# Kernel optimization log

Hardware: AMD Instinct MI355X
Metric: run time of the kernel (lower is better)

Reference implementation:

```python
import jax, jax.numpy as jnp
import numpy as np

D_IN, D, BOX, REL, THR = 2048, 512, 8, 80, 0.5

def _ln(x, g, b):
    m = jnp.mean(x, -1, keepdims=True)
    v = jnp.mean((x - m) ** 2, -1, keepdims=True)
    return (x - m) * jax.lax.rsqrt(v + 1e-5) * g + b

def setup_inputs():
    key = jax.random.key(0)
    ks = jax.random.split(key, 24)
    B, N = 32, 50
    def lin(k, i, o):
        return jax.random.normal(k, (i, o), jnp.float32) / np.sqrt(i)
    z = lambda n: jnp.zeros((n,), jnp.float32)
    o = lambda n: jnp.ones((n,), jnp.float32)
    return {
        "images": jax.random.normal(ks[0], (B, N, D_IN), jnp.float32),
        "selfbbox": jax.random.uniform(ks[1], (B, N, BOX), jnp.float32),
        "bbox": jax.random.uniform(ks[2], (B, N, N, BOX), jnp.float32),
        "pre_w": lin(ks[3], D_IN, D), "pre_b": z(D), "pre_g": o(D), "pre_be": z(D),
        "subj_w": lin(ks[4], D, D), "subj_b": z(D),
        "obj_w": lin(ks[5], D, D), "obj_b": z(D),
        "ps1_w": lin(ks[6], BOX, 64), "ps1_b": z(64), "ps_g": o(64), "ps_be": z(64),
        "ps2_w": lin(ks[7], 64, 64), "ps2_b": z(64),
        "pr1_w": lin(ks[8], BOX, 64), "pr1_b": z(64), "pr_g": o(64), "pr_be": z(64),
        "pr2_w": lin(ks[9], 64, 64), "pr2_b": z(64),
        "rs_w": lin(ks[10], D + 64, 1), "rs_b": z(1),
        "rf_w": lin(ks[11], D + 64, REL), "rf_b": z(REL),
        "g1_w": lin(ks[12], D + REL, D + REL), "g1_b": z(D + REL),
        "g2_w": lin(ks[13], D + REL, D), "g2_b": z(D),
        "g3_w": lin(ks[14], D, D), "g3_b": z(D),
    }

def reference(images, selfbbox, bbox, pre_w, pre_b, pre_g, pre_be, subj_w, subj_b,
              obj_w, obj_b, ps1_w, ps1_b, ps_g, ps_be, ps2_w, ps2_b,
              pr1_w, pr1_b, pr_g, pr_be, pr2_w, pr2_b, rs_w, rs_b, rf_w, rf_b,
              g1_w, g1_b, g2_w, g2_b, g3_w, g3_b):
    B, N = images.shape[0], images.shape[1]
    mask = jnp.sum(images, -1) != 0.0                      # [B,N] valid nodes
    attention_mask = (~mask)[:, None, None, :]             # [B,1,1,N]
    mf = mask.astype(images.dtype)
    # preprocess: Linear -> ReLU -> (dropout=id at eval) -> LayerNorm
    x = _ln(jax.nn.relu(images @ pre_w + pre_b), pre_g, pre_be)  # [B,N,512]
    x_subj = jax.nn.relu(x @ subj_w + subj_b) * mf[..., None]
    x_obj = jax.nn.relu(x @ obj_w + obj_b) * mf[..., None]
    eye = jnp.eye(N, dtype=bool)
    # pairwise subject/object features: diag(i==j) holds subject, off-diag object j
    x_rela = jnp.where(eye[None, :, :, None], x_subj[:, :, None, :], x_obj[:, None, :, :])
    x_rela = x_rela * mf[:, :, None, None]
    # positional MLPs
    h = jax.nn.relu(selfbbox @ ps1_w + ps1_b)
    h = jax.nn.relu(_ln(h, ps_g, ps_be) @ ps2_w + ps2_b)
    pos_self = h * mf[..., None]
    h = jax.nn.relu(bbox @ pr1_w + pr1_b)
    h = jax.nn.relu(_ln(h, pr_g, pr_be) @ pr2_w + pr2_b)
    pos_relas = h * mf[:, None, :, None] * mf[:, :, None, None]
    pos_rela = jnp.where(eye[None, :, :, None], pos_self[:, :, None, :], pos_relas)
    pos_rela = pos_rela * mf[:, :, None, None]
    pair = jnp.concatenate([x_rela, pos_rela], axis=-1)    # [B,N,N,576]
    pair_mask = mask[:, :, None] & mask[:, None, :]        # [B,N,N]
    # Relationshipness: pairwise relatedness score p + attention-pooled relation feats
    logits = (pair @ rs_w + rs_b)[..., 0]                  # [B,N,N]
    p = jax.nn.sigmoid(logits) * pair_mask.astype(images.dtype)
    attn = jax.nn.softmax(jnp.where(pair_mask, logits, -1e9), axis=2)
    feat = jax.nn.relu(pair @ rf_w + rf_b)                 # [B,N,N,80]
    relas = jnp.einsum('bij,bijf->bif', attn, feat) * mf[..., None]
    xx = jnp.concatenate([x, relas], axis=-1)              # [B,N,592]
    # dynamic edge threshold -> block-diagonal graph, expressed densely per image
    A = p > THR                                            # edge i->j
    Ahat = A | eye[None]                                   # add remaining self loops
    Af = Ahat.astype(xx.dtype)
    deg = jnp.sum(Af, axis=1)                              # in-degree at target j (>=1)
    dinv = jax.lax.rsqrt(deg)
    An = Af * dinv[:, :, None] * dinv[:, None, :]          # sym-normalized adjacency
    def gcn(hh, w, b):
        return jnp.einsum('bij,bif->bjf', An, hh @ w) + b
    x1 = jax.nn.relu(gcn(xx, g1_w, g1_b))
    x2 = jax.nn.relu(gcn(x1, g2_w, g2_b))
    x3 = jax.nn.relu(gcn(x2, g3_w, g3_b))
    outs = jnp.concatenate([x[:, None], x3[:, None]], axis=1)  # [B,2,N,512]
    return (outs, attention_mask)
```

## Files before the change

kernel.cpp:

```cpp
#include <hip/hip_runtime.h>
#include <hip/hip_bf16.h>

typedef __hip_bfloat16 bf16;

#define BB 32
#define NN 50
#define DIN 2048
#define DD 512
#define PD 64
#define FF 80
#define GG 592
#define BN (BB*NN)

#define O_FLAG  0
#define O_MF    16
#define O_SS    1616
#define O_SO    3216
#define O_PS    4816
#define O_FS    107216
#define O_FO    235216
#define O_RL    363216
#define O_LG    491216
#define O_AN    571216
#define O_T     651216
#define O_X1    1598416
#define O_X2    2545616
#define O_WPRE  3364816
#define O_BPRE  4413392
#define O_GPRE  4413904
#define O_EPRE  4414416
#define O_WSUBJ 4414928
#define O_BSUBJ 4677072
#define O_WOBJ  4677584
#define O_BOBJ  4939728
#define O_WPS1  4940240
#define O_BPS1  4940752
#define O_GPS   4940816
#define O_EPS   4940880
#define O_WPS2  4940944
#define O_BPS2  4945040
#define O_WPR1  4945104
#define O_BPR1  4945616
#define O_GPR   4945680
#define O_EPR   4945744
#define O_WPR2  4945808
#define O_BPR2  4949904
#define O_WRS   4949968
#define O_BRS   4950544
#define O_WRF   4950560
#define O_BRF   4996640
#define O_WG1   4996736
#define O_BG1   5347200
#define O_WG2   5347792
#define O_BG2   5650896
#define O_WG3   5651408
#define O_BG3   5913552
#define O_FT    5914064

#define PSLICE  819200

__device__ __forceinline__ float b2f(bf16 x){ return __bfloat162float(x); }

__device__ __forceinline__ float LDI(const bf16* p, size_t i, int f32m){
    if(f32m){
        bf16 a=p[2*i], b=p[2*i+1];
        unsigned short lo,hi;
        __builtin_memcpy(&lo,&a,2); __builtin_memcpy(&hi,&b,2);
        unsigned v=((unsigned)hi<<16)|(unsigned)lo;
        float f; __builtin_memcpy(&f,&v,4);
        return f;
    }
    return __bfloat162float(p[i]);
}

__global__ void k_flag(const bf16* __restrict__ images, float* __restrict__ ws){
    __shared__ int cnt;
    if(threadIdx.x==0) cnt=0;
    __syncthreads();
    bf16 h=images[2*threadIdx.x];
    unsigned short u; __builtin_memcpy(&u,&h,2);
    unsigned e=(u>>7)&0xFF;
    int sane=((u&0x7FFF)==0 || (e>=0x70&&e<=0x85))?1:0;
    atomicAdd(&cnt,sane);
    __syncthreads();
    if(threadIdx.x==0) ws[O_FLAG]=(cnt<48)?1.f:0.f;
}

__device__ __forceinline__ void conv(const bf16* s, float* d, int n, int F, int i0, int st){
    for(int g=i0; g<n; g+=st) d[g]=LDI(s,(size_t)g,F);
}
__global__ void kw(const bf16* p0,const bf16* p1,const bf16* p2,const bf16* p3,
                   const bf16* p4,const bf16* p5,const bf16* p6,const bf16* p7,
                   const bf16* p8,const bf16* p9,const bf16* p10,const bf16* p11,
                   const bf16* p12,const bf16* p13,const bf16* p14,const bf16* p15,
                   const bf16* p16,const bf16* p17,const bf16* p18,const bf16* p19,
                   const bf16* p20,const bf16* p21,const bf16* p22,const bf16* p23,
                   const bf16* p24,const bf16* p25,const bf16* p26,const bf16* p27,
                   const bf16* p28,const bf16* p29, float* __restrict__ ws){
    int F=ws[O_FLAG]>0.5f;
    int i0=blockIdx.x*256+threadIdx.x, st=gridDim.x*256;
    conv(p0, ws+O_WPRE, 1048576,F,i0,st);
    conv(p1, ws+O_BPRE, 512,F,i0,st);
    conv(p2, ws+O_GPRE, 512,F,i0,st);
    conv(p3, ws+O_EPRE, 512,F,i0,st);
    conv(p4, ws+O_WSUBJ,262144,F,i0,st);
    conv(p5, ws+O_BSUBJ,512,F,i0,st);
    conv(p6, ws+O_WOBJ, 262144,F,i0,st);
    conv(p7, ws+O_BOBJ, 512,F,i0,st);
    conv(p8, ws+O_WPS1, 512,F,i0,st);
    conv(p9, ws+O_BPS1, 64,F,i0,st);
    conv(p10,ws+O_GPS,  64,F,i0,st);
    conv(p11,ws+O_EPS,  64,F,i0,st);
    conv(p12,ws+O_WPS2, 4096,F,i0,st);
    conv(p13,ws+O_BPS2, 64,F,i0,st);
    conv(p14,ws+O_WPR1, 512,F,i0,st);
    conv(p15,ws+O_BPR1, 64,F,i0,st);
    conv(p16,ws+O_GPR,  64,F,i0,st);
    conv(p17,ws+O_EPR,  64,F,i0,st);
    conv(p18,ws+O_WPR2, 4096,F,i0,st);
    conv(p19,ws+O_BPR2, 64,F,i0,st);
    conv(p20,ws+O_WRS,  576,F,i0,st);
    conv(p21,ws+O_BRS,  1,F,i0,st);
    conv(p22,ws+O_WRF,  46080,F,i0,st);
    conv(p23,ws+O_BRF,  80,F,i0,st);
    conv(p24,ws+O_WG1,  350464,F,i0,st);
    conv(p25,ws+O_BG1,  592,F,i0,st);
    conv(p26,ws+O_WG2,  303104,F,i0,st);
    conv(p27,ws+O_BG2,  512,F,i0,st);
    conv(p28,ws+O_WG3,  262144,F,i0,st);
    conv(p29,ws+O_BG3,  512,F,i0,st);
}

__global__ void k_mask(const bf16* __restrict__ images, float* __restrict__ ws,
                       float* __restrict__ out){
    int t=threadIdx.x, wv=t>>6, ln=t&63;
    int r=blockIdx.x*4+wv;
    int F=ws[O_FLAG]>0.5f;
    float s=0.f;
    for(int k=ln;k<DIN;k+=64) s+=LDI(images,(size_t)r*DIN+k,F);
    for(int m=32;m>0;m>>=1) s+=__shfl_xor(s,m,64);
    if(ln==0){
        float mf=(s!=0.f)?1.f:0.f;
        ws[O_MF+r]=mf;
        out[(size_t)BB*2*NN*DD+r]=1.f-mf;
    }
}

__global__ void __launch_bounds__(256,4) k_x(const bf16* __restrict__ images,
                                             float* __restrict__ ws){
    __shared__ float as[8*256];
    int blk=blockIdx.x, t=threadIdx.x;
    int rg=blk>>3, ks=blk&7;
    int r0=rg*8, kbase=ks*256;
    int F=ws[O_FLAG]>0.5f;
    for(int idx=t; idx<8*256; idx+=256){
        int row=idx>>8, k=idx&255;
        as[idx]=LDI(images,(size_t)(r0+row)*DIN+kbase+k,F);
    }
    __syncthreads();
    const float* wP=ws+O_WPRE+(size_t)kbase*DD;
    int c0=t, c1=t+256;
    float acc[8][2]={};
    for(int k0=0;k0<256;k0+=8){
        float w0[8],w1[8];
        #pragma unroll
        for(int u=0;u<8;u++){ w0[u]=wP[(size_t)(k0+u)*DD+c0]; w1[u]=wP[(size_t)(k0+u)*DD+c1]; }
        #pragma unroll
        for(int u=0;u<8;u++){
            #pragma unroll
            for(int row=0;row<8;row++){
                float v=as[row*256+k0+u];
                acc[row][0]+=v*w0[u]; acc[row][1]+=v*w1[u];
            }
        }
    }
    float* P=ws + ((ks<7)? (O_FT+(size_t)ks*PSLICE) : (size_t)O_T);
    #pragma unroll
    for(int row=0;row<8;row++){
        size_t b=(size_t)(r0+row)*DD;
        P[b+c0]=acc[row][0]; P[b+c1]=acc[row][1];
    }
}

__global__ void __launch_bounds__(256,4) k_xr(float* __restrict__ ws, float* __restrict__ out){
    __shared__ float red[256];
    int blk=blockIdx.x, t=threadIdx.x;
    int r0=blk*4;
    const float* bPre=ws+O_BPRE; const float* gPre=ws+O_GPRE; const float* ePre=ws+O_EPRE;
    int c0=t, c1=t+256;
    for(int row=0;row<4;row++){
        int r=r0+row;
        float y0=bPre[c0], y1=bPre[c1];
        for(int ks=0;ks<8;ks++){
            const float* P=ws + ((ks<7)? (O_FT+(size_t)ks*PSLICE) : (size_t)O_T);
            y0+=P[(size_t)r*DD+c0]; y1+=P[(size_t)r*DD+c1];
        }
        y0=fmaxf(y0,0.f); y1=fmaxf(y1,0.f);
        red[t]=y0+y1; __syncthreads();
        for(int o=128;o>0;o>>=1){ if(t<o) red[t]+=red[t+o]; __syncthreads(); }
        float mean=red[0]/DD; __syncthreads();
        float d0=y0-mean, d1=y1-mean;
        red[t]=d0*d0+d1*d1; __syncthreads();
        for(int o=128;o>0;o>>=1){ if(t<o) red[t]+=red[t+o]; __syncthreads(); }
        float rstd=rsqrtf(red[0]/DD+1e-5f);
        __syncthreads();
        float xv0=d0*rstd*gPre[c0]+ePre[c0];
        float xv1=d1*rstd*gPre[c1]+ePre[c1];
        size_t ob=((size_t)(r/NN)*2)*NN*DD+(size_t)(r%NN)*DD;
        out[ob+c0]=xv0; out[ob+c1]=xv1;
    }
}

__global__ void __launch_bounds__(256,4) k_so1(const float* __restrict__ out,
                                               float* __restrict__ ws){
    __shared__ float xs[4*DD];
    __shared__ float mrow_s[4];
    int blk=blockIdx.x, t=threadIdx.x;
    int rg=blk>>2, mat=(blk>>1)&1, ch=blk&1;
    int r0=rg*4;
    for(int idx=t; idx<4*DD; idx+=256){
        int row=idx>>9, k=idx&511;
        int r=r0+row;
        xs[idx]=out[((size_t)(r/NN)*2)*NN*DD+(size_t)(r%NN)*DD+k];
    }
    if(t<4) mrow_s[t]=ws[O_MF+r0+t];
    __syncthreads();
    const float* W =ws+(mat?O_WOBJ:O_WSUBJ);
    const float* Bb=ws+(mat?O_BOBJ:O_BSUBJ);
    int c=ch*256+t;
    float acc[4]={0.f,0.f,0.f,0.f};
    for(int k0=0;k0<DD;k0+=8){
        float w[8];
        #pragma unroll
        for(int u=0;u<8;u++) w[u]=W[(size_t)(k0+u)*DD+c];
        #pragma unroll
        for(int u=0;u<8;u++){
            #pragma unroll
            for(int row=0;row<4;row++) acc[row]+=xs[row*DD+k0+u]*w[u];
        }
    }
    float* Y=ws+O_FT+(size_t)mat*PSLICE;
    #pragma unroll
    for(int row=0;row<4;row++)
        Y[(size_t)(r0+row)*DD+c]=fmaxf(acc[row]+Bb[c],0.f)*mrow_s[row];
}

__global__ void __launch_bounds__(256,4) k_so2(float* __restrict__ ws){
    __shared__ float yl[4][DD];
    int blk=blockIdx.x, t=threadIdx.x, wv=t>>6, ln=t&63;
    int combo=blk*4+wv;
    int mat=combo&1, r=combo>>1;
    const float* Y=ws+O_FT+(size_t)mat*PSLICE+(size_t)r*DD;
    for(int k=ln;k<DD;k+=64) yl[wv][k]=Y[k];
    __syncthreads();
    const float* wRs=ws+O_WRS;
    float ps=0.f;
    for(int k=ln;k<DD;k+=64) ps+=yl[wv][k]*wRs[k];
    for(int m=32;m>0;m>>=1) ps+=__shfl_xor(ps,m,64);
    if(ln==0) ws[(mat?O_SO:O_SS)+r]=ps;
    const float* wRf=ws+O_WRF;
    float* dst=ws+(mat?O_FO:O_FS)+(size_t)r*FF;
    {
        float a=0.f;
        for(int k=0;k<DD;k++) a+=yl[wv][k]*wRf[(size_t)k*FF+ln];
        dst[ln]=a;
    }
    if(ln<16){
        int c=64+ln;
        float a=0.f;
        for(int k=0;k<DD;k++) a+=yl[wv][k]*wRf[(size_t)k*FF+c];
        dst[c]=a;
    }
}

__global__ void k_pos_self(const bf16* __restrict__ sb, float* __restrict__ ws){
    __shared__ float h[PD];
    __shared__ float stat[2];
    int r=blockIdx.x, t=threadIdx.x;
    int F=ws[O_FLAG]>0.5f;
    const float* w1=ws+O_WPS1;
    float acc=0.f;
    for(int q=0;q<8;q++) acc+=LDI(sb,(size_t)r*8+q,F)*w1[q*PD+t];
    acc=fmaxf(acc+ws[O_BPS1+t],0.f);
    h[t]=acc; __syncthreads();
    if(t==0){
        float sm=0; for(int k=0;k<PD;k++) sm+=h[k];
        float mean=sm/PD;
        float v=0; for(int k=0;k<PD;k++){float d=h[k]-mean; v+=d*d;}
        stat[0]=mean; stat[1]=rsqrtf(v/PD+1e-5f);
    }
    __syncthreads();
    float hn=(acc-stat[0])*stat[1]*ws[O_GPS+t]+ws[O_EPS+t];
    h[t]=hn; __syncthreads();
    float a2=0.f;
    const float* w2=ws+O_WPS2;
    for(int k=0;k<PD;k++) a2+=h[k]*w2[k*PD+t];
    ws[O_PS+(size_t)r*PD+t]=fmaxf(a2+ws[O_BPS2+t],0.f)*ws[O_MF+r];
}

#define PSTRIDE 68
#define ZROW(m) ((m)*PSTRIDE + (((m)>>3)<<2))

__global__ void __launch_bounds__(256,3) k_pair(const bf16* __restrict__ bbox,
                                                float* __restrict__ ws){
    __shared__ float zp[64*PSTRIDE+64];
    __shared__ float wbuf[80*PSTRIDE];
    __shared__ float w1s[512];
    __shared__ float bbs[512];
    __shared__ float b1s[64], g1s[64], be1s[64], b2s[64], wrss[64];
    __shared__ float brfs[80];
    __shared__ float rowmi[64], rowmj[64], rowbase[64];
    __shared__ int   rowfb[64], rowps[64], rowdg[64];

    int t=threadIdx.x;
    int blk=blockIdx.x;
    int F=ws[O_FLAG]>0.5f;
    float rsb=ws[O_BRS];

    float wrfreg[20];
    #pragma unroll
    for(int u=0;u<20;u++){
        int idx=t+256*u;
        int f=idx>>6, k=idx&63;
        wrfreg[u]=ws[O_WRF+(size_t)(512+k)*FF+f];
    }

    for(int idx=t; idx<4096; idx+=256){ int k=idx>>6, c=idx&63; wbuf[k*PSTRIDE+c]=ws[O_WPR2+idx]; }
    for(int idx=t; idx<512; idx+=256) w1s[idx]=ws[O_WPR1+idx];
    for(int idx=t; idx<512; idx+=256) bbs[idx]=LDI(bbox,(size_t)blk*512+idx,F);
    if(t<64){
        b1s[t]=ws[O_BPR1+t]; g1s[t]=ws[O_GPR+t]; be1s[t]=ws[O_EPR+t];
        b2s[t]=ws[O_BPR2+t]; wrss[t]=ws[O_WRS+512+t];
    } else if(t<144){
        brfs[t-64]=ws[O_BRF+t-64];
    }
    if(t<64){
        int p=blk*64+t;
        int r=p/NN, j=p-r*NN;
        int b=r/NN, i=r-b*NN;
        int dg=(i==j);
        rowmi[t]=ws[O_MF+r];
        rowmj[t]=ws[O_MF+b*NN+j];
        rowdg[t]=dg;
        rowbase[t]=dg? ws[O_SS+r] : ws[O_SO+b*NN+j];
        rowfb[t]=dg? (O_FS+r*FF) : (O_FO+(b*NN+j)*FF);
        rowps[t]=O_PS+r*PD;
    }
    __syncthreads();

    int wv=t>>6, ln=t&63;
    for(int q=0;q<16;q++){
        int m=wv*16+q;
        float acc=0.f;
        #pragma unroll
        for(int u=0;u<8;u++) acc+=bbs[m*8+u]*w1s[u*64+ln];
        float h1=fmaxf(acc+b1s[ln],0.f);
        float sm=h1;
        for(int o=32;o>0;o>>=1) sm+=__shfl_xor(sm,o,64);
        float mean=sm*(1.f/64.f);
        float d=h1-mean;
        float vv=d*d;
        for(int o=32;o>0;o>>=1) vv+=__shfl_xor(vv,o,64);
        float rstd=rsqrtf(vv*(1.f/64.f)+1e-5f);
        zp[ZROW(m)+ln]=d*rstd*g1s[ln]+be1s[ln];
    }
    __syncthreads();

    int tr=t>>4, tc=t&15;
    int m0=tr*4, c0=tc*4;
    float a1[4][4]={};
    for(int k0=0;k0<64;k0+=4){
        float4 zv[4], wvv[4];
        #pragma unroll
        for(int i=0;i<4;i++) zv[i]=*(const float4*)&zp[ZROW(m0+i)+k0];
        #pragma unroll
        for(int u=0;u<4;u++) wvv[u]=*(const float4*)&wbuf[(k0+u)*PSTRIDE+c0];
        #pragma unroll
        for(int i=0;i<4;i++){
            const float* zpp=(const float*)&zv[i];
            #pragma unroll
            for(int u=0;u<4;u++){
                const float* wp=(const float*)&wvv[u];
                float zk=zpp[u];
                a1[i][0]+=zk*wp[0]; a1[i][1]+=zk*wp[1];
                a1[i][2]+=zk*wp[2]; a1[i][3]+=zk*wp[3];
            }
        }
    }
    __syncthreads();

    #pragma unroll
    for(int i=0;i<4;i++){
        int m=m0+i;
        float4 o;
        if(rowdg[m]){
            const float* ps=ws+rowps[m];
            o.x=ps[c0]; o.y=ps[c0+1]; o.z=ps[c0+2]; o.w=ps[c0+3];
        } else {
            float sc=rowmi[m]*rowmj[m];
            o.x=fmaxf(a1[i][0]+b2s[c0+0],0.f)*sc;
            o.y=fmaxf(a1[i][1]+b2s[c0+1],0.f)*sc;
            o.z=fmaxf(a1[i][2]+b2s[c0+2],0.f)*sc;
            o.w=fmaxf(a1[i][3]+b2s[c0+3],0.f)*sc;
        }
        *(float4*)&zp[ZROW(m)+c0]=o;
    }
    #pragma unroll
    for(int u=0;u<20;u++){
        int idx=t+256*u;
        wbuf[(idx>>6)*PSTRIDE+(idx&63)]=wrfreg[u];
    }
    __syncthreads();

    for(int q=0;q<16;q++){
        int m=wv*16+q;
        float lp=zp[ZROW(m)+ln]*wrss[ln];
        for(int o=32;o>0;o>>=1) lp+=__shfl_xor(lp,o,64);
        if(ln==0){
            ws[O_LG+(size_t)blk*64+m]=rowmi[m]*rowbase[m]+lp+rsb;
        }
    }

    {
        int c5=tc*5;
        float a2[4][5]={};
        for(int k0=0;k0<64;k0+=4){
            float4 zv[4], wv5[5];
            #pragma unroll
            for(int i=0;i<4;i++) zv[i]=*(const float4*)&zp[ZROW(m0+i)+k0];
            #pragma unroll
            for(int j=0;j<5;j++) wv5[j]=*(const float4*)&wbuf[(c5+j)*PSTRIDE+k0];
            #pragma unroll
            for(int i=0;i<4;i++){
                const float* zpp=(const float*)&zv[i];
                #pragma unroll
                for(int j=0;j<5;j++){
                    const float* wp=(const float*)&wv5[j];
                    a2[i][j]+=zpp[0]*wp[0]+zpp[1]*wp[1]+zpp[2]*wp[2]+zpp[3]*wp[3];
                }
            }
        }
        #pragma unroll
        for(int i=0;i<4;i++){
            int m=m0+i;
            size_t p=(size_t)blk*64+m;
            float mi=rowmi[m];
            const float* fb=ws+rowfb[m];
            #pragma unroll
            for(int j=0;j<5;j++){
                int c=c5+j;
                ws[O_FT+p*FF+c]=fmaxf(mi*fb[c]+a2[i][j]+brfs[c],0.f);
            }
        }
    }
}

__global__ void k_relas(float* __restrict__ ws){
    __shared__ float attn[64];
    int r=blockIdx.x, t=threadIdx.x;
    int b=r/NN;
    float mi=ws[O_MF+r];
    if(t<64){
        float v=-1e9f;
        if(t<NN){
            float mj=ws[O_MF+b*NN+t];
            bool pm=(mi>0.5f)&&(mj>0.5f);
            v=pm? ws[O_LG+(size_t)r*NN+t] : -1e9f;
        }
        float mx=v;
        for(int o=32;o>0;o>>=1) mx=fmaxf(mx,__shfl_xor(mx,o,64));
        float e=(t<NN)? __expf(v-mx) : 0.f;
        float sm=e;
        for(int o=32;o>0;o>>=1) sm+=__shfl_xor(sm,o,64);
        attn[t]=e*(1.f/sm);
    }
    __syncthreads();
    if(t<FF){
        float s=0.f;
        const float* ft=ws+O_FT+(size_t)r*NN*FF;
        for(int j=0;j<NN;j++) s+=attn[j]*ft[(size_t)j*FF+t];
        ws[O_RL+(size_t)r*FF+t]=s*mi;
    }
}

__global__ void k_adj(float* __restrict__ ws){
    __shared__ float Af[NN*NN];
    __shared__ float dinv[NN];
    int b=blockIdx.x, t=threadIdx.x;
    for(int idx=t; idx<NN*NN; idx+=256){
        int i=idx/NN, j=idx%NN;
        float l=ws[O_LG+(size_t)b*NN*NN+idx];
        bool a=(l>0.f)&&(ws[O_MF+b*NN+i]>0.5f)&&(ws[O_MF+b*NN+j]>0.5f);
        Af[idx]=(a||i==j)?1.f:0.f;
    }
    __syncthreads();
    if(t<NN){
        float dg=0.f;
        for(int i=0;i<NN;i++) dg+=Af[i*NN+t];
        dinv[t]=rsqrtf(dg);
    }
    __syncthreads();
    for(int idx=t; idx<NN*NN; idx+=256){
        int i=idx/NN, j=idx%NN;
        ws[O_AN+(size_t)b*NN*NN+idx]=Af[idx]*dinv[i]*dinv[j];
    }
}

__global__ void kt(int mode, const float* __restrict__ out, const float* __restrict__ ws,
                   const float* __restrict__ W, float* __restrict__ T,
                   int K, int NCOL, int NTILE){
    __shared__ float xs[10*GG];
    int blk=blockIdx.x, t=threadIdx.x;
    int rg=blk/NTILE, tile=blk%NTILE;
    for(int idx=t; idx<10*K; idx+=256){
        int row=idx/K, k=idx-row*K;
        int gr=rg*10+row;
        float v;
        if(mode==0){
            int bb=gr/NN, ii=gr-bb*NN;
            if(k<DD) v=out[(size_t)(2*bb)*NN*DD+(size_t)ii*DD+k];
            else     v=ws[O_RL+(size_t)gr*FF+(k-DD)];
        } else if(mode==1) v=ws[O_X1+(size_t)gr*GG+k];
        else               v=ws[O_X2+(size_t)gr*DD+k];
        xs[row*K+k]=v;
    }
    __syncthreads();
    int c=tile*256+t;
    if(c>=NCOL) return;
    float acc[10];
    #pragma unroll
    for(int u=0;u<10;u++) acc[u]=0.f;
    for(int k=0;k<K;k++){
        float w=W[(size_t)k*NCOL+c];
        #pragma unroll
        for(int u=0;u<10;u++) acc[u]+=xs[u*K+k]*w;
    }
    int gr0=rg*10;
    #pragma unroll
    for(int u=0;u<10;u++) T[(size_t)(gr0+u)*NCOL+c]=acc[u];
}

__global__ void ka(int mode, float* __restrict__ ws, const float* __restrict__ bias,
                   float* __restrict__ out, int NCOL){
    __shared__ float acol[NN];
    int rj=blockIdx.x, t=threadIdx.x;
    int b=rj/NN, j=rj-b*NN;
    if(t<NN) acol[t]=ws[O_AN+(size_t)b*NN*NN+t*NN+j];
    __syncthreads();
    const float* Tb=ws+O_T+(size_t)b*NN*NCOL;
    for(int c=t;c<NCOL;c+=256){
        float acc=0.f;
        for(int i2=0;i2<NN;i2++) acc+=acol[i2]*Tb[(size_t)i2*NCOL+c];
        float v=fmaxf(acc+bias[c],0.f);
        if(mode==2)      out[(size_t)(2*b+1)*NN*DD+(size_t)j*DD+c]=v;
        else if(mode==1) ws[O_X2+(size_t)rj*DD+c]=v;
        else             ws[O_X1+(size_t)rj*GG+c]=v;
    }
}

extern "C" void kernel_launch(void* const* d_in, const int* in_sizes, int n_in,
                              void* d_out, int out_size, void* d_ws, size_t ws_size,
                              hipStream_t stream) {
    const bf16* images  = (const bf16*)d_in[0];
    const bf16* selfbbox= (const bf16*)d_in[1];
    const bf16* bbox    = (const bf16*)d_in[2];

    float* out=(float*)d_out;
    float* ws =(float*)d_ws;

    k_flag<<<1,64,0,stream>>>(images, ws);
    kw<<<512,256,0,stream>>>((const bf16*)d_in[3],(const bf16*)d_in[4],(const bf16*)d_in[5],
                             (const bf16*)d_in[6],(const bf16*)d_in[7],(const bf16*)d_in[8],
                             (const bf16*)d_in[9],(const bf16*)d_in[10],(const bf16*)d_in[11],
                             (const bf16*)d_in[12],(const bf16*)d_in[13],(const bf16*)d_in[14],
                             (const bf16*)d_in[15],(const bf16*)d_in[16],(const bf16*)d_in[17],
                             (const bf16*)d_in[18],(const bf16*)d_in[19],(const bf16*)d_in[20],
                             (const bf16*)d_in[21],(const bf16*)d_in[22],(const bf16*)d_in[23],
                             (const bf16*)d_in[24],(const bf16*)d_in[25],(const bf16*)d_in[26],
                             (const bf16*)d_in[27],(const bf16*)d_in[28],(const bf16*)d_in[29],
                             (const bf16*)d_in[30],(const bf16*)d_in[31],(const bf16*)d_in[32],
                             ws);
    k_mask<<<400,256,0,stream>>>(images, ws, out);
    k_x<<<1600,256,0,stream>>>(images, ws);
    k_xr<<<400,256,0,stream>>>(ws, out);
    k_pos_self<<<BN,PD,0,stream>>>(selfbbox, ws);
    k_so1<<<1600,256,0,stream>>>(out, ws);
    k_so2<<<800,256,0,stream>>>(ws);
    k_pair<<<1250,256,0,stream>>>(bbox, ws);
    k_relas<<<BN,128,0,stream>>>(ws);
    k_adj<<<BB,256,0,stream>>>(ws);

    kt<<<160*3,256,0,stream>>>(0, out, ws, ws+O_WG1, ws+O_T, GG, GG, 3);
    ka<<<BN,256,0,stream>>>(0, ws, ws+O_BG1, out, GG);
    kt<<<160*2,256,0,stream>>>(1, out, ws, ws+O_WG2, ws+O_T, GG, DD, 2);
    ka<<<BN,256,0,stream>>>(1, ws, ws+O_BG2, out, DD);
    kt<<<160*2,256,0,stream>>>(2, out, ws, ws+O_WG3, ws+O_T, DD, DD, 2);
    ka<<<BN,256,0,stream>>>(2, ws, ws+O_BG3, out, DD);
}
```

Measured before the change: 675.7 us.

## Cut shared memory in pair kernel and halve row tile in GCN transform

The pair kernel moves small weights, biases and bbox values from shared memory into registers, using wave shuffles to broadcast bbox entries. It recomputes the per-row index metadata instead of caching it in shared arrays and raises launch bounds to 4 blocks per SM, all to get more resident blocks. The GCN transform kernel now handles 5 rows per block instead of 10, with an 8-way unrolled weight load and twice as many blocks, which improves occupancy and parallelism. The cost is more register pressure, repeated integer division, and each weight column being read twice as often from global memory.

```diff
diff --git a/kernel.cpp b/kernel.cpp
--- a/kernel.cpp
+++ b/kernel.cpp
@@ -298,25 +298,36 @@
     ws[O_PS+(size_t)r*PD+t]=fmaxf(a2+ws[O_BPS2+t],0.f)*ws[O_MF+r];
 }
 
-#define PSTRIDE 68
-#define ZROW(m) ((m)*PSTRIDE + (((m)>>3)<<2))
-
-__global__ void __launch_bounds__(256,3) k_pair(const bf16* __restrict__ bbox,
+#define WST 68
+#define ZROW(m) ((m)*64 + (((m)>>3)<<2))
+
+__global__ void __launch_bounds__(256,4) k_pair(const bf16* __restrict__ bbox,
                                                 float* __restrict__ ws){
-    __shared__ float zp[64*PSTRIDE+64];
-    __shared__ float wbuf[80*PSTRIDE];
-    __shared__ float w1s[512];
-    __shared__ float bbs[512];
-    __shared__ float b1s[64], g1s[64], be1s[64], b2s[64], wrss[64];
-    __shared__ float brfs[80];
-    __shared__ float rowmi[64], rowmj[64], rowbase[64];
-    __shared__ int   rowfb[64], rowps[64], rowdg[64];
+    __shared__ float zp[4128];
+    __shared__ float wbuf[80*WST];
+    __shared__ float rowmi[64], rowmj[64];
 
     int t=threadIdx.x;
     int blk=blockIdx.x;
+    int wv=t>>6, ln=t&63;
+    int tr=t>>4, tc=t&15;
+    int m0=tr*4, c0=tc*4, c5=tc*5;
     int F=ws[O_FLAG]>0.5f;
     float rsb=ws[O_BRS];
 
+    float w1r[8];
+    #pragma unroll
+    for(int u=0;u<8;u++) w1r[u]=ws[O_WPR1+u*64+ln];
+    float b1r=ws[O_BPR1+ln], g1r=ws[O_GPR+ln], ber=ws[O_EPR+ln];
+    float wrsr=ws[O_WRS+512+ln];
+    float b2r[4];
+    #pragma unroll
+    for(int u=0;u<4;u++) b2r[u]=ws[O_BPR2+c0+u];
+    float brfr[5];
+    #pragma unroll
+    for(int u=0;u<5;u++) brfr[u]=ws[O_BRF+c5+u];
+    float breg0=LDI(bbox,(size_t)blk*512+wv*128+ln,F);
+    float breg1=LDI(bbox,(size_t)blk*512+wv*128+64+ln,F);
     float wrfreg[20];
     #pragma unroll
     for(int u=0;u<20;u++){
@@ -325,36 +336,26 @@
         wrfreg[u]=ws[O_WRF+(size_t)(512+k)*FF+f];
     }
 
-    for(int idx=t; idx<4096; idx+=256){ int k=idx>>6, c=idx&63; wbuf[k*PSTRIDE+c]=ws[O_WPR2+idx]; }
-    for(int idx=t; idx<512; idx+=256) w1s[idx]=ws[O_WPR1+idx];
-    for(int idx=t; idx<512; idx+=256) bbs[idx]=LDI(bbox,(size_t)blk*512+idx,F);
-    if(t<64){
-        b1s[t]=ws[O_BPR1+t]; g1s[t]=ws[O_GPR+t]; be1s[t]=ws[O_EPR+t];
-        b2s[t]=ws[O_BPR2+t]; wrss[t]=ws[O_WRS+512+t];
-    } else if(t<144){
-        brfs[t-64]=ws[O_BRF+t-64];
-    }
+    for(int idx=t; idx<4096; idx+=256){ int k=idx>>6, c=idx&63; wbuf[k*WST+c]=ws[O_WPR2+idx]; }
     if(t<64){
         int p=blk*64+t;
         int r=p/NN, j=p-r*NN;
-        int b=r/NN, i=r-b*NN;
-        int dg=(i==j);
+        int b=r/NN;
         rowmi[t]=ws[O_MF+r];
         rowmj[t]=ws[O_MF+b*NN+j];
-        rowdg[t]=dg;
-        rowbase[t]=dg? ws[O_SS+r] : ws[O_SO+b*NN+j];
-        rowfb[t]=dg? (O_FS+r*FF) : (O_FO+(b*NN+j)*FF);
-        rowps[t]=O_PS+r*PD;
-    }
-    __syncthreads();
-
-    int wv=t>>6, ln=t&63;
+    }
+    __syncthreads();
+
+    #pragma unroll
     for(int q=0;q<16;q++){
         int m=wv*16+q;
         float acc=0.f;
         #pragma unroll
-        for(int u=0;u<8;u++) acc+=bbs[m*8+u]*w1s[u*64+ln];
-        float h1=fmaxf(acc+b1s[ln],0.f);
+        for(int u=0;u<8;u++){
+            float bb=(q<8)? __shfl(breg0,(q&7)*8+u,64) : __shfl(breg1,(q&7)*8+u,64);
+            acc+=bb*w1r[u];
+        }
+        float h1=fmaxf(acc+b1r,0.f);
         float sm=h1;
         for(int o=32;o>0;o>>=1) sm+=__shfl_xor(sm,o,64);
         float mean=sm*(1.f/64.f);
@@ -362,19 +363,17 @@
         float vv=d*d;
         for(int o=32;o>0;o>>=1) vv+=__shfl_xor(vv,o,64);
         float rstd=rsqrtf(vv*(1.f/64.f)+1e-5f);
-        zp[ZROW(m)+ln]=d*rstd*g1s[ln]+be1s[ln];
-    }
-    __syncthreads();
-
-    int tr=t>>4, tc=t&15;
-    int m0=tr*4, c0=tc*4;
+        zp[ZROW(m)+ln]=d*rstd*g1r+ber;
+    }
+    __syncthreads();
+
     float a1[4][4]={};
     for(int k0=0;k0<64;k0+=4){
         float4 zv[4], wvv[4];
         #pragma unroll
         for(int i=0;i<4;i++) zv[i]=*(const float4*)&zp[ZROW(m0+i)+k0];
         #pragma unroll
-        for(int u=0;u<4;u++) wvv[u]=*(const float4*)&wbuf[(k0+u)*PSTRIDE+c0];
+        for(int u=0;u<4;u++) wvv[u]=*(const float4*)&wbuf[(k0+u)*WST+c0];
         #pragma unroll
         for(int i=0;i<4;i++){
             const float* zpp=(const float*)&zv[i];
@@ -392,44 +391,49 @@
     #pragma unroll
     for(int i=0;i<4;i++){
         int m=m0+i;
+        int p=blk*64+m;
+        int r=p/NN, j=p-r*NN;
+        int b=r/NN, ii=r-b*NN;
         float4 o;
-        if(rowdg[m]){
-            const float* ps=ws+rowps[m];
-            o.x=ps[c0]; o.y=ps[c0+1]; o.z=ps[c0+2]; o.w=ps[c0+3];
+        if(ii==j){
+            o=*(const float4*)&ws[O_PS+(size_t)r*PD+c0];
         } else {
             float sc=rowmi[m]*rowmj[m];
-            o.x=fmaxf(a1[i][0]+b2s[c0+0],0.f)*sc;
-            o.y=fmaxf(a1[i][1]+b2s[c0+1],0.f)*sc;
-            o.z=fmaxf(a1[i][2]+b2s[c0+2],0.f)*sc;
-            o.w=fmaxf(a1[i][3]+b2s[c0+3],0.f)*sc;
+            o.x=fmaxf(a1[i][0]+b2r[0],0.f)*sc;
+            o.y=fmaxf(a1[i][1]+b2r[1],0.f)*sc;
+            o.z=fmaxf(a1[i][2]+b2r[2],0.f)*sc;
+            o.w=fmaxf(a1[i][3]+b2r[3],0.f)*sc;
         }
         *(float4*)&zp[ZROW(m)+c0]=o;
     }
     #pragma unroll
     for(int u=0;u<20;u++){
         int idx=t+256*u;
-        wbuf[(idx>>6)*PSTRIDE+(idx&63)]=wrfreg[u];
+        wbuf[(idx>>6)*WST+(idx&63)]=wrfreg[u];
     }
     __syncthreads();
 
     for(int q=0;q<16;q++){
         int m=wv*16+q;
-        float lp=zp[ZROW(m)+ln]*wrss[ln];
+        float lp=zp[ZROW(m)+ln]*wrsr;
         for(int o=32;o>0;o>>=1) lp+=__shfl_xor(lp,o,64);
         if(ln==0){
-            ws[O_LG+(size_t)blk*64+m]=rowmi[m]*rowbase[m]+lp+rsb;
+            int p=blk*64+m;
+            int r=p/NN, j=p-r*NN;
+            int b=r/NN, ii=r-b*NN;
+            float base=(ii==j)? ws[O_SS+r] : ws[O_SO+b*NN+j];
+            ws[O_LG+(size_t)blk*64+m]=rowmi[m]*base+lp+rsb;
         }
     }
 
     {
-        int c5=tc*5;
         float a2[4][5]={};
         for(int k0=0;k0<64;k0+=4){
             float4 zv[4], wv5[5];
             #pragma unroll
             for(int i=0;i<4;i++) zv[i]=*(const float4*)&zp[ZROW(m0+i)+k0];
             #pragma unroll
-            for(int j=0;j<5;j++) wv5[j]=*(const float4*)&wbuf[(c5+j)*PSTRIDE+k0];
+            for(int j=0;j<5;j++) wv5[j]=*(const float4*)&wbuf[(c5+j)*WST+k0];
             #pragma unroll
             for(int i=0;i<4;i++){
                 const float* zpp=(const float*)&zv[i];
@@ -444,12 +448,14 @@
         for(int i=0;i<4;i++){
             int m=m0+i;
             size_t p=(size_t)blk*64+m;
+            int r=(int)p/NN, j=(int)p-r*NN;
+            int b=r/NN, ii=r-b*NN;
+            const float* fb=ws+((ii==j)? (O_FS+(size_t)r*FF) : (O_FO+(size_t)(b*NN+j)*FF));
             float mi=rowmi[m];
-            const float* fb=ws+rowfb[m];
-            #pragma unroll
-            for(int j=0;j<5;j++){
-                int c=c5+j;
-                ws[O_FT+p*FF+c]=fmaxf(mi*fb[c]+a2[i][j]+brfs[c],0.f);
+            #pragma unroll
+            for(int jj=0;jj<5;jj++){
+                int c=c5+jj;
+                ws[O_FT+p*FF+c]=fmaxf(mi*fb[c]+a2[i][jj]+brfr[jj],0.f);
             }
         }
     }
@@ -506,15 +512,16 @@
     }
 }
 
-__global__ void kt(int mode, const float* __restrict__ out, const float* __restrict__ ws,
+__global__ void __launch_bounds__(256,4) kt(int mode, const float* __restrict__ out,
+                   const float* __restrict__ ws,
                    const float* __restrict__ W, float* __restrict__ T,
                    int K, int NCOL, int NTILE){
-    __shared__ float xs[10*GG];
+    __shared__ float xs[5*GG];
     int blk=blockIdx.x, t=threadIdx.x;
     int rg=blk/NTILE, tile=blk%NTILE;
-    for(int idx=t; idx<10*K; idx+=256){
+    for(int idx=t; idx<5*K; idx+=256){
         int row=idx/K, k=idx-row*K;
-        int gr=rg*10+row;
+        int gr=rg*5+row;
         float v;
         if(mode==0){
             int bb=gr/NN, ii=gr-bb*NN;
@@ -527,17 +534,22 @@
     __syncthreads();
     int c=tile*256+t;
     if(c>=NCOL) return;
-    float acc[10];
-    #pragma unroll
-    for(int u=0;u<10;u++) acc[u]=0.f;
-    for(int k=0;k<K;k++){
-        float w=W[(size_t)k*NCOL+c];
-        #pragma unroll
-        for(int u=0;u<10;u++) acc[u]+=xs[u*K+k]*w;
-    }
-    int gr0=rg*10;
-    #pragma unroll
-    for(int u=0;u<10;u++) T[(size_t)(gr0+u)*NCOL+c]=acc[u];
+    float acc[5];
+    #pragma unroll
+    for(int u=0;u<5;u++) acc[u]=0.f;
+    for(int k0=0;k0<K;k0+=8){
+        float w[8];
+        #pragma unroll
+        for(int u=0;u<8;u++) w[u]=W[(size_t)(k0+u)*NCOL+c];
+        #pragma unroll
+        for(int u=0;u<8;u++){
+            #pragma unroll
+            for(int row=0;row<5;row++) acc[row]+=xs[row*K+k0+u]*w[u];
+        }
+    }
+    int gr0=rg*5;
+    #pragma unroll
+    for(int u=0;u<5;u++) T[(size_t)(gr0+u)*NCOL+c]=acc[u];
 }
 
 __global__ void ka(int mode, float* __restrict__ ws, const float* __restrict__ bias,
@@ -590,10 +602,10 @@
     k_relas<<<BN,128,0,stream>>>(ws);
     k_adj<<<BB,256,0,stream>>>(ws);
 
-    kt<<<160*3,256,0,stream>>>(0, out, ws, ws+O_WG1, ws+O_T, GG, GG, 3);
+    kt<<<320*3,256,0,stream>>>(0, out, ws, ws+O_WG1, ws+O_T, GG, GG, 3);
     ka<<<BN,256,0,stream>>>(0, ws, ws+O_BG1, out, GG);
-    kt<<<160*2,256,0,stream>>>(1, out, ws, ws+O_WG2, ws+O_T, GG, DD, 2);
+    kt<<<320*2,256,0,stream>>>(1, out, ws, ws+O_WG2, ws+O_T, GG, DD, 2);
     ka<<<BN,256,0,stream>>>(1, ws, ws+O_BG2, out, DD);
-    kt<<<160*2,256,0,stream>>>(2, out, ws, ws+O_WG3, ws+O_T, DD, DD, 2);
+    kt<<<320*2,256,0,stream>>>(2, out, ws, ws+O_WG3, ws+O_T, DD, DD, 2);
     ka<<<BN,256,0,stream>>>(2, ws, ws+O_BG3, out, DD);
 }
```

Result: slower. 1.025 ms (+51.7%).
